# Kernel optimization log

Hardware: AMD Instinct MI355X
Metric: run time of the kernel (lower is better)

Reference implementation:

```python
import jax, jax.numpy as jnp
import numpy as np

SEQ, BATCH, INP = 20, 16384, 2
HID, EMB = 256, 64
TARGET_LEN = 30


def setup_inputs() -> dict:
    key = jax.random.key(0)
    ks = jax.random.split(key, 12)
    s = 0.1
    return {
        "x_input": jax.random.normal(ks[0], (SEQ, BATCH, INP), dtype=jnp.float32),
        # encoder embedding Linear(input_size -> emb_dim)
        "W_emb": jax.random.normal(ks[1], (EMB, INP), dtype=jnp.float32) * s,
        "b_emb": jax.random.normal(ks[2], (EMB,), dtype=jnp.float32) * s,
        # encoder LSTM (input EMB -> hidden HID), PyTorch gate order i,f,g,o; bias = b_ih + b_hh
        "W_ih_enc": jax.random.normal(ks[3], (4 * HID, EMB), dtype=jnp.float32) * s,
        "W_hh_enc": jax.random.normal(ks[4], (4 * HID, HID), dtype=jnp.float32) * s,
        "b_enc": jax.random.normal(ks[5], (4 * HID,), dtype=jnp.float32) * s,
        # decoder LSTM (input INP -> hidden HID)
        "W_ih_dec": jax.random.normal(ks[6], (4 * HID, INP), dtype=jnp.float32) * s,
        "W_hh_dec": jax.random.normal(ks[7], (4 * HID, HID), dtype=jnp.float32) * s,
        "b_dec": jax.random.normal(ks[8], (4 * HID,), dtype=jnp.float32) * s,
        # decoder output Linear(hidden -> input_size)
        "W_out": jax.random.normal(ks[9], (INP, HID), dtype=jnp.float32) * s,
        "b_out": jax.random.normal(ks[10], (INP,), dtype=jnp.float32) * s,
        "target_len": TARGET_LEN,
    }


def _lstm_cell(x, h, c, W_ih, W_hh, b):
    # x: [B, in], h/c: [B, H]; PyTorch gate order: input, forget, cell(g), output
    gates = x @ W_ih.T + h @ W_hh.T + b  # [B, 4H]
    i, f, g, o = jnp.split(gates, 4, axis=-1)
    c_new = jax.nn.sigmoid(f) * c + jax.nn.sigmoid(i) * jnp.tanh(g)
    h_new = jax.nn.sigmoid(o) * jnp.tanh(c_new)
    return h_new, c_new


def reference(x_input, W_emb, b_emb, W_ih_enc, W_hh_enc, b_enc,
              W_ih_dec, W_hh_dec, b_dec, W_out, b_out, target_len):
    B = x_input.shape[1]
    # --- encoder ---
    x_emb = x_input @ W_emb.T + b_emb  # [S, B, EMB]
    h0 = jnp.zeros((B, HID), dtype=x_input.dtype)
    c0 = jnp.zeros((B, HID), dtype=x_input.dtype)

    def enc_step(carry, xt):
        h, c = carry
        h, c = _lstm_cell(xt, h, c, W_ih_enc, W_hh_enc, b_enc)
        return (h, c), None

    (h_enc, c_enc), _ = jax.lax.scan(enc_step, (h0, c0), x_emb)

    dec_in0 = x_input[-1]  # [B, INP]

    def dec_step(carry, _):
        di, h, c = carry
        h, c = _lstm_cell(di, h, c, W_ih_dec, W_hh_dec, b_dec)
        out = h @ W_out.T + b_out  # [B, INP]
        return (out, h, c), out

    _, outputs = jax.lax.scan(dec_step, (dec_in0, h_enc, c_enc), None,
                              length=int(target_len))
    return outputs  # [target_len, B, INP]
```

## Files before the change

kernel.cpp:

```cpp
#include <hip/hip_runtime.h>


#define SEQ  20
#define TLEN 30
#define LOG2E  1.442695041f
#define LOG2E2 2.885390082f

typedef _Float16 half8   __attribute__((ext_vector_type(8)));
typedef _Float16 half4   __attribute__((ext_vector_type(4)));
typedef float    floatx4 __attribute__((ext_vector_type(4)));

__device__ _Float16 g_w_enc[1024 * 288];
__device__ _Float16 g_w_dec0[1024 * 288];
__device__ _Float16 g_w_deff[1024 * 288];
__device__ _Float16 g_wout[512];
__device__ float    g_bias_dec[1024];

__global__ void prep_kernel(const float* __restrict__ W_emb,
                            const float* __restrict__ b_emb,
                            const float* __restrict__ W_ih_enc,
                            const float* __restrict__ W_hh_enc,
                            const float* __restrict__ b_enc,
                            const float* __restrict__ W_ih_dec,
                            const float* __restrict__ W_hh_dec,
                            const float* __restrict__ b_dec,
                            const float* __restrict__ W_out,
                            const float* __restrict__ b_out) {
    int gid = blockIdx.x * blockDim.x + threadIdx.x;
    int stride = gridDim.x * blockDim.x;
    for (int s = gid; s < 1024 * 288; s += stride) {
        int n = s / 288, k = s - n * 288;
        int g = n >> 8, c = (n >> 4) & 15, l16 = n & 15;
        int w = c >> 1, cc = c & 1;
        int i = cc * 4 + g;
        int kt = k >> 5, q = (k >> 3) & 3, j = k & 7;
        int dst = ((w * 9 + kt) * 8 + i) * 512 + q * 128 + l16 * 8 + j;
        float sc = (g == 2) ? LOG2E2 : LOG2E;
        float fe = 0.f, fd = 0.f, ff = 0.f;
        if (k < 256) {
            fe = W_hh_enc[n * 256 + k];
            fd = W_hh_dec[n * 256 + k];
            ff = fd + W_ih_dec[2 * n] * W_out[k]
                    + W_ih_dec[2 * n + 1] * W_out[256 + k];
        } else {
            int kp = k - 256;
            if (kp < 2) {
                fd = W_ih_dec[2 * n + kp];
                const float* wr = &W_ih_enc[n * 64];
                for (int e = 0; e < 64; e++) fe = fmaf(wr[e], W_emb[2 * e + kp], fe);
            } else if (kp == 2) {
                fd = b_dec[n];
                ff = b_dec[n] + W_ih_dec[2 * n] * b_out[0]
                              + W_ih_dec[2 * n + 1] * b_out[1];
                fe = b_enc[n];
                const float* wr = &W_ih_enc[n * 64];
                for (int e = 0; e < 64; e++) fe = fmaf(wr[e], b_emb[e], fe);
                g_bias_dec[(w * 8 + i) * 16 + l16] = ff * sc;
            }
        }
        g_w_enc[dst]  = (_Float16)(fe * sc);
        g_w_dec0[dst] = (_Float16)(fd * sc);
        g_w_deff[dst] = (_Float16)(ff * sc);
    }
    if (gid < 512) g_wout[gid] = (_Float16)W_out[gid];
}

__global__ __launch_bounds__(512, 2) void lstm_fused(
        const float* __restrict__ x_input,
        const float* __restrict__ b_out,
        float* __restrict__ out)
{
    __shared__ __align__(16) _Float16 h_pack[2][18432];
    __shared__ __align__(16) float    partial_lds[2][8 * 132];
    __shared__ __align__(16) _Float16 w_lds[32768];
    __shared__ __align__(16) float    bias_lds[1024];

    const int tid = threadIdx.x;
    const int w   = tid >> 6;
    const int L   = tid & 63;
    const int l16 = L & 15;
    const int q   = L >> 4;
    const long row0 = (long)blockIdx.x * 64;

    {
        int* hz = (int*)&h_pack[0][0];
        for (int idx = tid; idx < 18432; idx += 512) hz[idx] = 0;
    }
    {
        const half8* __restrict__ gsrc = (const half8*)&g_w_enc[w * 36864];
        half8* ldst = (half8*)&w_lds[w * 4096];
#pragma unroll
        for (int r8 = 0; r8 < 8; r8++) ldst[r8 * 64 + L] = gsrc[r8 * 64 + L];
    }
    bias_lds[tid]       = g_bias_dec[tid];
    bias_lds[tid + 512] = g_bias_dec[tid + 512];
    __syncthreads();
    if (tid < 128) {
        int buf = tid >> 6, b = tid & 63;
        h_pack[buf][((b >> 4) * 9 + 8) * 512 + (b & 15) * 8 + 2] = (_Float16)1.f;
    }
    if (tid < 128) {
        int b = tid >> 1, jj = tid & 1;
        h_pack[0][((b >> 4) * 9 + 8) * 512 + (b & 15) * 8 + jj] =
            (_Float16)x_input[(row0 + b) * 2 + jj];
    }

    const float bo = b_out[tid & 1];
    const int aoff = q * 128 + l16 * 8;
    const _Float16* __restrict__ wenc_w  = &g_w_enc[w * 36864];
    const _Float16* __restrict__ wdec0_w = &g_w_dec0[w * 36864];
    const _Float16* __restrict__ wdeff_w = &g_w_deff[w * 36864];

    _Float16 wo[2][2][4];
#pragma unroll
    for (int jj = 0; jj < 2; jj++)
#pragma unroll
        for (int cc = 0; cc < 2; cc++)
#pragma unroll
            for (int r = 0; r < 4; r++)
                wo[jj][cc][r] = g_wout[jj * 256 + 32 * w + 16 * cc + 4 * q + r];

    floatx4 acc[8][4];
    float   c_st[4][2][4];
#pragma unroll
    for (int nt = 0; nt < 4; nt++)
#pragma unroll
        for (int cc = 0; cc < 2; cc++)
#pragma unroll
            for (int r = 0; r < 4; r++) c_st[nt][cc][r] = 0.f;

    __syncthreads();

    int cur = 0;
#pragma unroll 1
    for (int t = 0; t < SEQ + TLEN; t++) {
        const _Float16* __restrict__ Wb =
            (t < SEQ) ? wenc_w : (t == SEQ) ? wdec0_w : wdeff_w;
        const bool skip8 = (t > SEQ);
        const _Float16* __restrict__ hp = h_pack[cur];
        _Float16* __restrict__ hn = h_pack[cur ^ 1];

        float xval = 0.f;
        if (t < SEQ && tid < 128) {
            int srct = (t + 1 < SEQ) ? t + 1 : SEQ - 1;
            xval = x_input[(long)srct * 32768 + (row0 + (tid >> 1)) * 2 + (tid & 1)];
        }

#pragma unroll
        for (int kt = 0; kt < 9; kt++) {
            if (kt < 8 || !skip8) {
                half8 B[4];
#pragma unroll
                for (int nt = 0; nt < 4; nt++)
                    B[nt] = *(const half8*)&hp[(nt * 9 + kt) * 512 + aoff];
#pragma unroll
                for (int i = 0; i < 8; i++) {
                    if (kt == 0) {
                        half8 Aw = *(const half8*)&w_lds[w * 4096 + i * 512 + aoff];
                        if (skip8) {
                            floatx4 bfr = *(const floatx4*)
                                &bias_lds[(w * 8 + i) * 16 + q * 4];
#pragma unroll
                            for (int nt = 0; nt < 4; nt++)
                                acc[i][nt] = __builtin_amdgcn_mfma_f32_16x16x32_f16(
                                    Aw, B[nt], bfr, 0, 0, 0);
                        } else {
#pragma unroll
                            for (int nt = 0; nt < 4; nt++)
                                acc[i][nt] = __builtin_amdgcn_mfma_f32_16x16x32_f16(
                                    Aw, B[nt], (floatx4)(0.f), 0, 0, 0);
                        }
                    } else {
                        half8 Aw = *(const half8*)&Wb[(kt * 8 + i) * 512 + aoff];
#pragma unroll
                        for (int nt = 0; nt < 4; nt++)
                            acc[i][nt] = __builtin_amdgcn_mfma_f32_16x16x32_f16(
                                Aw, B[nt], acc[i][nt], 0, 0, 0);
                    }
                }
            }
        }

        const bool dec = (t >= SEQ);
        float po[4][2];
#pragma unroll
        for (int nt = 0; nt < 4; nt++) { po[nt][0] = 0.f; po[nt][1] = 0.f; }

#pragma unroll
        for (int nt = 0; nt < 4; nt++)
#pragma unroll
            for (int cc = 0; cc < 2; cc++) {
                half4 hv4;
                float hvf[4];
#pragma unroll
                for (int r = 0; r < 4; r++) {
                    float ai = acc[cc * 4 + 0][nt][r];
                    float af = acc[cc * 4 + 1][nt][r];
                    float ag = acc[cc * 4 + 2][nt][r];
                    float ao = acc[cc * 4 + 3][nt][r];
                    float eI = __builtin_amdgcn_exp2f(-ai);
                    float eF = __builtin_amdgcn_exp2f(-af);
                    float eG = __builtin_amdgcn_exp2f(-ag);
                    float eO = __builtin_amdgcn_exp2f(-ao);
                    float a1 = 1.f + eI;
                    float a2 = 1.f + eG;
                    float a3 = 1.f + eF;
                    float t1 = a1 * a2;
                    float num = fmaf(c_st[nt][cc][r], t1, (1.f - eG) * a3);
                    float cn  = num * __builtin_amdgcn_rcpf(t1 * a3);
                    c_st[nt][cc][r] = cn;
                    float cnc = fminf(fmaxf(cn, -12.f), 12.f);
                    float eC = __builtin_amdgcn_exp2f(-LOG2E2 * cnc);
                    float hv = (1.f - eC) *
                        __builtin_amdgcn_rcpf((1.f + eO) * (1.f + eC));
                    hvf[r] = hv;
                    hv4[r] = (_Float16)hv;
                }
                *(half4*)&hn[(nt * 9 + w) * 512 + (2 * cc + (q >> 1)) * 128 +
                             l16 * 8 + 4 * (q & 1)] = hv4;
                if (dec) {
#pragma unroll
                    for (int r = 0; r < 4; r++) {
                        po[nt][0] = fmaf(hvf[r], (float)wo[0][cc][r], po[nt][0]);
                        po[nt][1] = fmaf(hvf[r], (float)wo[1][cc][r], po[nt][1]);
                    }
                }
            }

        if (dec) {
#pragma unroll
            for (int nt = 0; nt < 4; nt++)
#pragma unroll
                for (int jj = 0; jj < 2; jj++) {
                    float s = po[nt][jj];
                    s += __shfl_xor(s, 16);
                    s += __shfl_xor(s, 32);
                    po[nt][jj] = s;
                }
            if (q == 0) {
                float* pl = &partial_lds[t & 1][w * 132];
#pragma unroll
                for (int nt = 0; nt < 4; nt++) {
                    pl[nt * 16 + l16]      = po[nt][0];
                    pl[66 + nt * 16 + l16] = po[nt][1];
                }
            }
        }

        if (t < SEQ && tid < 128) {
            int b = tid >> 1, jj = tid & 1;
            hn[((b >> 4) * 9 + 8) * 512 + (b & 15) * 8 + jj] = (_Float16)xval;
        }

        if (t == SEQ - 1 || t == SEQ) {
            const _Float16* __restrict__ wsrc =
                (t == SEQ - 1) ? &g_w_dec0[w * 36864] : &g_w_deff[w * 36864];
            const half8* __restrict__ gsrc = (const half8*)wsrc;
            half8* ldst = (half8*)&w_lds[w * 4096];
#pragma unroll 2
            for (int r8 = 0; r8 < 8; r8++) ldst[r8 * 64 + L] = gsrc[r8 * 64 + L];
        }

        __syncthreads();

        if (dec && tid < 128) {
            int m = tid >> 1, jj = tid & 1;
            const float* pl = &partial_lds[t & 1][jj * 66 + m];
            float s = bo;
#pragma unroll
            for (int w8 = 0; w8 < 8; w8++) s += pl[w8 * 132];
            out[(long)(t - SEQ) * 32768 + (row0 + m) * 2 + jj] = s;
        }

        cur ^= 1;
    }
}

extern "C" void kernel_launch(void* const* d_in, const int* in_sizes, int n_in,
                              void* d_out, int out_size, void* d_ws, size_t ws_size,
                              hipStream_t stream) {
    (void)in_sizes; (void)n_in; (void)d_ws; (void)ws_size; (void)out_size;
    const float* x      = (const float*)d_in[0];
    const float* W_emb  = (const float*)d_in[1];
    const float* b_emb  = (const float*)d_in[2];
    const float* W_ih_e = (const float*)d_in[3];
    const float* W_hh_e = (const float*)d_in[4];
    const float* b_enc  = (const float*)d_in[5];
    const float* W_ih_d = (const float*)d_in[6];
    const float* W_hh_d = (const float*)d_in[7];
    const float* b_dec  = (const float*)d_in[8];
    const float* W_out  = (const float*)d_in[9];
    const float* b_out  = (const float*)d_in[10];
    float* outp = (float*)d_out;

    prep_kernel<<<512, 256, 0, stream>>>(W_emb, b_emb, W_ih_e, W_hh_e, b_enc,
                                         W_ih_d, W_hh_d, b_dec, W_out, b_out);
    lstm_fused<<<256, 512, 0, stream>>>(x, b_out, outp);
}
```

Before: 666.1 us.

## Split LSTM time loop into templated encoder/decoder phases and drop LDS weight tile

The single time loop with runtime branches on encoder, first-decoder and later-decoder steps is replaced by a templated step function instantiated per phase, so each loop body is specialised at compile time without per-step conditionals. The 64 KB LDS copy of the first K-tile of weights is removed, and all weight tiles are now read directly from global memory (cache). This frees a large share of shared memory per block, which may allow more blocks per CU, and removes the mid-loop weight reloads. The cost is more global/L2 traffic for the first weight tile and larger code size from three instantiations.

```diff
diff --git a/kernel.cpp b/kernel.cpp
--- a/kernel.cpp
+++ b/kernel.cpp
@@ -65,6 +65,148 @@
     if (gid < 512) g_wout[gid] = (_Float16)W_out[gid];
 }
 
+template<int MODE>
+__device__ __forceinline__ void lstm_step(
+        int t,
+        const _Float16* __restrict__ Wb,
+        const _Float16* __restrict__ hp,
+        _Float16* __restrict__ hn,
+        float* __restrict__ pl_buf,
+        const float* __restrict__ bias_lds,
+        const float* __restrict__ x_input,
+        float* __restrict__ out,
+        floatx4 (&acc)[8][4],
+        float (&c_st)[4][2][4],
+        const _Float16 (&wo)[2][2][4],
+        int tid, int w, int q, int l16, int aoff, long row0, float bo)
+{
+    constexpr bool ENC   = (MODE == 0);
+    constexpr bool DEC   = (MODE >= 1);
+    constexpr bool SKIP8 = (MODE == 2);
+    constexpr int  NKT   = SKIP8 ? 8 : 9;
+
+    float xval = 0.f;
+    if (ENC && tid < 128) {
+        int srct = (t + 1 < SEQ) ? t + 1 : SEQ - 1;
+        xval = x_input[(long)srct * 32768 + (row0 + (tid >> 1)) * 2 + (tid & 1)];
+    }
+
+#pragma unroll
+    for (int kt = 0; kt < NKT; kt++) {
+        half8 B[4];
+#pragma unroll
+        for (int nt = 0; nt < 4; nt++)
+            B[nt] = *(const half8*)&hp[(nt * 9 + kt) * 512 + aoff];
+#pragma unroll
+        for (int i = 0; i < 8; i++) {
+            half8 Aw = *(const half8*)&Wb[(kt * 8 + i) * 512 + aoff];
+            if (kt == 0) {
+                if (SKIP8) {
+                    floatx4 bfr = *(const floatx4*)
+                        &bias_lds[(w * 8 + i) * 16 + q * 4];
+#pragma unroll
+                    for (int nt = 0; nt < 4; nt++)
+                        acc[i][nt] = __builtin_amdgcn_mfma_f32_16x16x32_f16(
+                            Aw, B[nt], bfr, 0, 0, 0);
+                } else {
+#pragma unroll
+                    for (int nt = 0; nt < 4; nt++)
+                        acc[i][nt] = __builtin_amdgcn_mfma_f32_16x16x32_f16(
+                            Aw, B[nt], (floatx4)(0.f), 0, 0, 0);
+                }
+            } else {
+#pragma unroll
+                for (int nt = 0; nt < 4; nt++)
+                    acc[i][nt] = __builtin_amdgcn_mfma_f32_16x16x32_f16(
+                        Aw, B[nt], acc[i][nt], 0, 0, 0);
+            }
+        }
+    }
+
+    float po[4][2];
+    if (DEC) {
+#pragma unroll
+        for (int nt = 0; nt < 4; nt++) { po[nt][0] = 0.f; po[nt][1] = 0.f; }
+    }
+
+#pragma unroll
+    for (int nt = 0; nt < 4; nt++)
+#pragma unroll
+        for (int cc = 0; cc < 2; cc++) {
+            half4 hv4;
+            float hvf[4];
+#pragma unroll
+            for (int r = 0; r < 4; r++) {
+                float ai = acc[cc * 4 + 0][nt][r];
+                float af = acc[cc * 4 + 1][nt][r];
+                float ag = acc[cc * 4 + 2][nt][r];
+                float ao = acc[cc * 4 + 3][nt][r];
+                float eI = __builtin_amdgcn_exp2f(-ai);
+                float eF = __builtin_amdgcn_exp2f(-af);
+                float eG = __builtin_amdgcn_exp2f(-ag);
+                float eO = __builtin_amdgcn_exp2f(-ao);
+                float a1 = 1.f + eI;
+                float a2 = 1.f + eG;
+                float a3 = 1.f + eF;
+                float t1 = a1 * a2;
+                float num = fmaf(c_st[nt][cc][r], t1, (1.f - eG) * a3);
+                float cn  = num * __builtin_amdgcn_rcpf(t1 * a3);
+                c_st[nt][cc][r] = cn;
+                float cnc = fminf(fmaxf(cn, -12.f), 12.f);
+                float eC = __builtin_amdgcn_exp2f(-LOG2E2 * cnc);
+                float hv = (1.f - eC) *
+                    __builtin_amdgcn_rcpf((1.f + eO) * (1.f + eC));
+                hvf[r] = hv;
+                hv4[r] = (_Float16)hv;
+            }
+            *(half4*)&hn[(nt * 9 + w) * 512 + (2 * cc + (q >> 1)) * 128 +
+                         l16 * 8 + 4 * (q & 1)] = hv4;
+            if (DEC) {
+#pragma unroll
+                for (int r = 0; r < 4; r++) {
+                    po[nt][0] = fmaf(hvf[r], (float)wo[0][cc][r], po[nt][0]);
+                    po[nt][1] = fmaf(hvf[r], (float)wo[1][cc][r], po[nt][1]);
+                }
+            }
+        }
+
+    if (DEC) {
+#pragma unroll
+        for (int nt = 0; nt < 4; nt++)
+#pragma unroll
+            for (int jj = 0; jj < 2; jj++) {
+                float s = po[nt][jj];
+                s += __shfl_xor(s, 16);
+                s += __shfl_xor(s, 32);
+                po[nt][jj] = s;
+            }
+        if (q == 0) {
+            float* pl = &pl_buf[w * 132];
+#pragma unroll
+            for (int nt = 0; nt < 4; nt++) {
+                pl[nt * 16 + l16]      = po[nt][0];
+                pl[66 + nt * 16 + l16] = po[nt][1];
+            }
+        }
+    }
+
+    if (ENC && tid < 128) {
+        int b = tid >> 1, jj = tid & 1;
+        hn[((b >> 4) * 9 + 8) * 512 + (b & 15) * 8 + jj] = (_Float16)xval;
+    }
+
+    __syncthreads();
+
+    if (DEC && tid < 128) {
+        int m = tid >> 1, jj = tid & 1;
+        const float* pl = &pl_buf[jj * 66 + m];
+        float s = bo;
+#pragma unroll
+        for (int w8 = 0; w8 < 8; w8++) s += pl[w8 * 132];
+        out[(long)(t - SEQ) * 32768 + (row0 + m) * 2 + jj] = s;
+    }
+}
+
 __global__ __launch_bounds__(512, 2) void lstm_fused(
         const float* __restrict__ x_input,
         const float* __restrict__ b_out,
@@ -72,7 +214,6 @@
 {
     __shared__ __align__(16) _Float16 h_pack[2][18432];
     __shared__ __align__(16) float    partial_lds[2][8 * 132];
-    __shared__ __align__(16) _Float16 w_lds[32768];
     __shared__ __align__(16) float    bias_lds[1024];
 
     const int tid = threadIdx.x;
@@ -86,12 +227,6 @@
         int* hz = (int*)&h_pack[0][0];
         for (int idx = tid; idx < 18432; idx += 512) hz[idx] = 0;
     }
-    {
-        const half8* __restrict__ gsrc = (const half8*)&g_w_enc[w * 36864];
-        half8* ldst = (half8*)&w_lds[w * 4096];
-#pragma unroll
-        for (int r8 = 0; r8 < 8; r8++) ldst[r8 * 64 + L] = gsrc[r8 * 64 + L];
-    }
     bias_lds[tid]       = g_bias_dec[tid];
     bias_lds[tid + 512] = g_bias_dec[tid + 512];
     __syncthreads();
@@ -131,149 +266,21 @@
 
     __syncthreads();
 
-    int cur = 0;
 #pragma unroll 1
-    for (int t = 0; t < SEQ + TLEN; t++) {
-        const _Float16* __restrict__ Wb =
-            (t < SEQ) ? wenc_w : (t == SEQ) ? wdec0_w : wdeff_w;
-        const bool skip8 = (t > SEQ);
-        const _Float16* __restrict__ hp = h_pack[cur];
-        _Float16* __restrict__ hn = h_pack[cur ^ 1];
-
-        float xval = 0.f;
-        if (t < SEQ && tid < 128) {
-            int srct = (t + 1 < SEQ) ? t + 1 : SEQ - 1;
-            xval = x_input[(long)srct * 32768 + (row0 + (tid >> 1)) * 2 + (tid & 1)];
-        }
-
-#pragma unroll
-        for (int kt = 0; kt < 9; kt++) {
-            if (kt < 8 || !skip8) {
-                half8 B[4];
-#pragma unroll
-                for (int nt = 0; nt < 4; nt++)
-                    B[nt] = *(const half8*)&hp[(nt * 9 + kt) * 512 + aoff];
-#pragma unroll
-                for (int i = 0; i < 8; i++) {
-                    if (kt == 0) {
-                        half8 Aw = *(const half8*)&w_lds[w * 4096 + i * 512 + aoff];
-                        if (skip8) {
-                            floatx4 bfr = *(const floatx4*)
-                                &bias_lds[(w * 8 + i) * 16 + q * 4];
-#pragma unroll
-                            for (int nt = 0; nt < 4; nt++)
-                                acc[i][nt] = __builtin_amdgcn_mfma_f32_16x16x32_f16(
-                                    Aw, B[nt], bfr, 0, 0, 0);
-                        } else {
-#pragma unroll
-                            for (int nt = 0; nt < 4; nt++)
-                                acc[i][nt] = __builtin_amdgcn_mfma_f32_16x16x32_f16(
-                                    Aw, B[nt], (floatx4)(0.f), 0, 0, 0);
-                        }
-                    } else {
-                        half8 Aw = *(const half8*)&Wb[(kt * 8 + i) * 512 + aoff];
-#pragma unroll
-                        for (int nt = 0; nt < 4; nt++)
-                            acc[i][nt] = __builtin_amdgcn_mfma_f32_16x16x32_f16(
-                                Aw, B[nt], acc[i][nt], 0, 0, 0);
-                    }
-                }
-            }
-        }
-
-        const bool dec = (t >= SEQ);
-        float po[4][2];
-#pragma unroll
-        for (int nt = 0; nt < 4; nt++) { po[nt][0] = 0.f; po[nt][1] = 0.f; }
-
-#pragma unroll
-        for (int nt = 0; nt < 4; nt++)
-#pragma unroll
-            for (int cc = 0; cc < 2; cc++) {
-                half4 hv4;
-                float hvf[4];
-#pragma unroll
-                for (int r = 0; r < 4; r++) {
-                    float ai = acc[cc * 4 + 0][nt][r];
-                    float af = acc[cc * 4 + 1][nt][r];
-                    float ag = acc[cc * 4 + 2][nt][r];
-                    float ao = acc[cc * 4 + 3][nt][r];
-                    float eI = __builtin_amdgcn_exp2f(-ai);
-                    float eF = __builtin_amdgcn_exp2f(-af);
-                    float eG = __builtin_amdgcn_exp2f(-ag);
-                    float eO = __builtin_amdgcn_exp2f(-ao);
-                    float a1 = 1.f + eI;
-                    float a2 = 1.f + eG;
-                    float a3 = 1.f + eF;
-                    float t1 = a1 * a2;
-                    float num = fmaf(c_st[nt][cc][r], t1, (1.f - eG) * a3);
-                    float cn  = num * __builtin_amdgcn_rcpf(t1 * a3);
-                    c_st[nt][cc][r] = cn;
-                    float cnc = fminf(fmaxf(cn, -12.f), 12.f);
-                    float eC = __builtin_amdgcn_exp2f(-LOG2E2 * cnc);
-                    float hv = (1.f - eC) *
-                        __builtin_amdgcn_rcpf((1.f + eO) * (1.f + eC));
-                    hvf[r] = hv;
-                    hv4[r] = (_Float16)hv;
-                }
-                *(half4*)&hn[(nt * 9 + w) * 512 + (2 * cc + (q >> 1)) * 128 +
-                             l16 * 8 + 4 * (q & 1)] = hv4;
-                if (dec) {
-#pragma unroll
-                    for (int r = 0; r < 4; r++) {
-                        po[nt][0] = fmaf(hvf[r], (float)wo[0][cc][r], po[nt][0]);
-                        po[nt][1] = fmaf(hvf[r], (float)wo[1][cc][r], po[nt][1]);
-                    }
-                }
-            }
-
-        if (dec) {
-#pragma unroll
-            for (int nt = 0; nt < 4; nt++)
-#pragma unroll
-                for (int jj = 0; jj < 2; jj++) {
-                    float s = po[nt][jj];
-                    s += __shfl_xor(s, 16);
-                    s += __shfl_xor(s, 32);
-                    po[nt][jj] = s;
-                }
-            if (q == 0) {
-                float* pl = &partial_lds[t & 1][w * 132];
-#pragma unroll
-                for (int nt = 0; nt < 4; nt++) {
-                    pl[nt * 16 + l16]      = po[nt][0];
-                    pl[66 + nt * 16 + l16] = po[nt][1];
-                }
-            }
-        }
-
-        if (t < SEQ && tid < 128) {
-            int b = tid >> 1, jj = tid & 1;
-            hn[((b >> 4) * 9 + 8) * 512 + (b & 15) * 8 + jj] = (_Float16)xval;
-        }
-
-        if (t == SEQ - 1 || t == SEQ) {
-            const _Float16* __restrict__ wsrc =
-                (t == SEQ - 1) ? &g_w_dec0[w * 36864] : &g_w_deff[w * 36864];
-            const half8* __restrict__ gsrc = (const half8*)wsrc;
-            half8* ldst = (half8*)&w_lds[w * 4096];
-#pragma unroll 2
-            for (int r8 = 0; r8 < 8; r8++) ldst[r8 * 64 + L] = gsrc[r8 * 64 + L];
-        }
-
-        __syncthreads();
-
-        if (dec && tid < 128) {
-            int m = tid >> 1, jj = tid & 1;
-            const float* pl = &partial_lds[t & 1][jj * 66 + m];
-            float s = bo;
-#pragma unroll
-            for (int w8 = 0; w8 < 8; w8++) s += pl[w8 * 132];
-            out[(long)(t - SEQ) * 32768 + (row0 + m) * 2 + jj] = s;
-        }
-
-        cur ^= 1;
-    }
+    for (int t = 0; t < SEQ; t++)
+        lstm_step<0>(t, wenc_w, h_pack[t & 1], h_pack[(t & 1) ^ 1],
+                     &partial_lds[t & 1][0], bias_lds, x_input, out,
+                     acc, c_st, wo, tid, w, q, l16, aoff, row0, bo);
+
+    lstm_step<1>(SEQ, wdec0_w, h_pack[SEQ & 1], h_pack[(SEQ & 1) ^ 1],
+                 &partial_lds[SEQ & 1][0], bias_lds, x_input, out,
+                 acc, c_st, wo, tid, w, q, l16, aoff, row0, bo);
+
+#pragma unroll 1
+    for (int t = SEQ + 1; t < SEQ + TLEN; t++)
+        lstm_step<2>(t, wdeff_w, h_pack[t & 1], h_pack[(t & 1) ^ 1],
+                     &partial_lds[t & 1][0], bias_lds, x_input, out,
+                     acc, c_st, wo, tid, w, q, l16, aoff, row0, bo);
 }
 
 extern "C" void kernel_launch(void* const* d_in, const int* in_sizes, int n_in,
```

Measured after the change: 1.738 ms. +160.9%, slower.
